# Kernel optimization log

Hardware: AMD Instinct MI355X
Metric: run time of the kernel (lower is better)

## Reference

```python
import jax, jax.numpy as jnp
import numpy as np

# Model dims (match init_kwargs)
U, I, E = 100000, 50000, 1000000   # users, items, interactions
FD, EK, EF = 64, 64, 64            # feature_dim, embed_k, embed_f
L = 3                              # n_layers
B = 16384                          # scoring batch
ALPHA = [1.0 / (k + 1) for k in range(L + 1)]


def setup_inputs() -> dict:
    key = jax.random.key(0)
    ks = jax.random.split(key, 9)
    Gu = jax.random.normal(ks[0], (U, EK), jnp.float32) * 0.05
    Gi = jax.random.normal(ks[1], (I, EK), jnp.float32) * 0.05
    F = jax.random.normal(ks[2], (FD, EF), jnp.float32) * 0.1
    proj_w = jax.random.normal(ks[3], (EF, 1), jnp.float32) * 0.1
    proj_b = jnp.zeros((1,), jnp.float32)
    # sparse binary-ish decomposition-path feature matrix (dense here)
    edge_features = (jax.random.uniform(ks[4], (E, FD)) < 0.1).astype(jnp.float32)
    u = jax.random.randint(ks[5], (E,), 0, U)
    it = jax.random.randint(ks[6], (E,), 0, I) + U  # items offset by num_users
    edge_index = jnp.stack([jnp.concatenate([u, it]),
                            jnp.concatenate([it, u])]).astype(jnp.int64)  # [2, 2E]
    users = jax.random.randint(ks[7], (B,), 0, U).astype(jnp.int64)
    items = jax.random.randint(ks[8], (B,), 0, I).astype(jnp.int64)
    return dict(Gu=Gu, Gi=Gi, F=F, proj_w=proj_w, proj_b=proj_b,
                edge_features=edge_features, edge_index=edge_index,
                users=users, items=items)


def _propagate(Gu, Gi, F, proj_w, proj_b, edge_features, edge_index):
    N = U + I
    src, dst = edge_index[0], edge_index[1]
    # edge-feature projection -> scalar edge weight, duplicated per direction
    ew = (edge_features @ F) @ proj_w + proj_b            # [E, 1]
    ew = jnp.concatenate([ew, ew], axis=0)[:, 0]          # [2E]
    # symmetric GCN normalization over the bipartite interaction graph
    deg = jax.ops.segment_sum(jnp.ones_like(ew), dst, num_segments=N)  # [N]
    dinv = jnp.where(deg > 0, jax.lax.rsqrt(jnp.maximum(deg, 1.0)), 0.0)
    coef = (dinv[src] * dinv[dst] * ew)[:, None]          # [2E, 1]
    x = jnp.concatenate([Gu, Gi], axis=0)                 # [N, K]
    out = ALPHA[0] * x
    for k in range(L):  # edge-conditioned gather -> scale -> scatter-add
        x = jax.ops.segment_sum(coef * x[src], dst, num_segments=N)
        out = out + ALPHA[k + 1] * x
    return out[:U], out[U:]


def reference(Gu, Gi, F, proj_w, proj_b, edge_features, edge_index, users, items):
    gu, gi = _propagate(Gu, Gi, F, proj_w, proj_b, edge_features, edge_index)
    # forward(): masked dot-product scoring of (user, item) pairs
    return jnp.sum(gu[users] * gi[items], axis=1)  # [B]
```

## Files before the change

### kernel.cpp

```cpp
#include <hip/hip_runtime.h>

constexpr int Uc = 100000;
constexpr int Ic = 50000;
constexpr int Nc = 150000;
constexpr int Ec = 1000000;
constexpr int Bc = 16384;
constexpr int NBS = (Nc + 1023) / 1024;

typedef _Float16 h16;
union H4 { uint2 u; h16 h[4]; };


__global__ void k_zero(uint4* __restrict__ deg4) {
    int i = blockIdx.x * blockDim.x + threadIdx.x;
    if (i < Nc / 4) deg4[i] = make_uint4(0u, 0u, 0u, 0u);
}

__global__ void k_deg2_fproj(const int* __restrict__ un, const int* __restrict__ in_,
                             unsigned* __restrict__ deg,
                             const float* __restrict__ F, const float* __restrict__ pw,
                             float* __restrict__ Fp) {
    if (blockIdx.x == 0 && threadIdx.x < 64) {
        int d = threadIdx.x;
        float s = 0.f;
#pragma unroll
        for (int j = 0; j < 64; ++j) s += F[d * 64 + j] * pw[j];
        Fp[d] = s;
    }
    int e = blockIdx.x * blockDim.x + threadIdx.x;
    if (e < Ec) {
        atomicAdd(&deg[un[e]], 1u);
        atomicAdd(&deg[in_[e]], 1u);
    }
}

__global__ void k_scan1(const unsigned* __restrict__ deg, int* __restrict__ rowptr,
                        int* __restrict__ bsums, float* __restrict__ dinv) {
    __shared__ int sh[256];
    int tid = threadIdx.x, bid = blockIdx.x;
    int base = bid * 1024 + tid * 4;
    int v0 = (base + 0 < Nc) ? (int)deg[base + 0] : 0;
    int v1 = (base + 1 < Nc) ? (int)deg[base + 1] : 0;
    int v2 = (base + 2 < Nc) ? (int)deg[base + 2] : 0;
    int v3 = (base + 3 < Nc) ? (int)deg[base + 3] : 0;
    if (base + 0 < Nc) dinv[base + 0] = v0 ? rsqrtf((float)v0) : 0.f;
    if (base + 1 < Nc) dinv[base + 1] = v1 ? rsqrtf((float)v1) : 0.f;
    if (base + 2 < Nc) dinv[base + 2] = v2 ? rsqrtf((float)v2) : 0.f;
    if (base + 3 < Nc) dinv[base + 3] = v3 ? rsqrtf((float)v3) : 0.f;
    int s = v0 + v1 + v2 + v3;
    sh[tid] = s;
    __syncthreads();
    for (int off = 1; off < 256; off <<= 1) {
        int t = (tid >= off) ? sh[tid - off] : 0;
        __syncthreads();
        sh[tid] += t;
        __syncthreads();
    }
    int excl = sh[tid] - s;
    if (tid == 255) bsums[bid] = sh[255];
    if (base + 0 < Nc) rowptr[base + 0] = excl;
    if (base + 1 < Nc) rowptr[base + 1] = excl + v0;
    if (base + 2 < Nc) rowptr[base + 2] = excl + v0 + v1;
    if (base + 3 < Nc) rowptr[base + 3] = excl + v0 + v1 + v2;
}

__global__ void k_scan3(int* __restrict__ rowptr, const int* __restrict__ bsums,
                        int* __restrict__ cursor) {
    __shared__ int sh[256];
    int tid = threadIdx.x;
    int v = (tid < NBS) ? bsums[tid] : 0;
    sh[tid] = v;
    __syncthreads();
    for (int off = 1; off < 256; off <<= 1) {
        int t = (tid >= off) ? sh[tid - off] : 0;
        __syncthreads();
        sh[tid] += t;
        __syncthreads();
    }
    int excl = sh[tid] - v;
    __syncthreads();
    sh[tid] = excl;
    __syncthreads();
    int i = blockIdx.x * blockDim.x + threadIdx.x;
    if (i < Nc) {
        int r = rowptr[i] + sh[i >> 10];
        rowptr[i] = r;
        cursor[i] = r;
    }
    if (i == 0) rowptr[Nc] = 2 * Ec;
}

__global__ void k_build(const int* __restrict__ un, const int* __restrict__ in_,
                        const float* __restrict__ ef, const float* __restrict__ Fp,
                        const float* __restrict__ pb, const float* __restrict__ dinv,
                        int* __restrict__ cursor, int2* __restrict__ csr) {
    int t = blockIdx.x * blockDim.x + threadIdx.x;
    int e = t >> 4, l = t & 15;
    if (e >= Ec) return;
    float4 f = reinterpret_cast<const float4*>(ef)[(size_t)e * 16 + l];
    float4 w = reinterpret_cast<const float4*>(Fp)[l];
    float s = f.x * w.x + f.y * w.y + f.z * w.z + f.w * w.w;
    s += __shfl_xor(s, 8, 16);
    s += __shfl_xor(s, 4, 16);
    s += __shfl_xor(s, 2, 16);
    s += __shfl_xor(s, 1, 16);
    if (l == 0 || l == 8) {
        int uu = un[e], ii = in_[e];
        float c = dinv[uu] * dinv[ii] * (s + pb[0]);
        if (l == 0) {
            int pos = atomicAdd(&cursor[ii], 1);
            csr[pos] = make_int2(uu, __float_as_int(c));
        } else {
            int pos = atomicAdd(&cursor[uu], 1);
            csr[pos] = make_int2(ii, __float_as_int(c));
        }
    }
}

__global__ void k_xin(const float* __restrict__ Gu, const float* __restrict__ Gi,
                      uint2* __restrict__ xin) {
    int t = blockIdx.x * blockDim.x + threadIdx.x;
    if (t >= Nc * 16) return;
    float4 v = (t < Uc * 16) ? reinterpret_cast<const float4*>(Gu)[t]
                             : reinterpret_cast<const float4*>(Gi)[t - Uc * 16];
    H4 o;
    o.h[0] = (h16)v.x; o.h[1] = (h16)v.y; o.h[2] = (h16)v.z; o.h[3] = (h16)v.w;
    xin[t] = o.u;
}

__global__ void k_gprop(const int* __restrict__ rowptr, const int2* __restrict__ csr,
                        const uint2* __restrict__ x, uint2* __restrict__ xn) {
    int t = blockIdx.x * blockDim.x + threadIdx.x;
    int n = t >> 4, l = t & 15;
    if (n >= Nc) return;
    int e0 = rowptr[n], e1 = rowptr[n + 1];
    float4 acc = make_float4(0.f, 0.f, 0.f, 0.f);
    int e = e0;
    for (; e + 4 <= e1; e += 4) {
        int2 s0 = csr[e], s1 = csr[e + 1], s2 = csr[e + 2], s3 = csr[e + 3];
        H4 v0, v1, v2, v3;
        v0.u = x[s0.x * 16 + l];
        v1.u = x[s1.x * 16 + l];
        v2.u = x[s2.x * 16 + l];
        v3.u = x[s3.x * 16 + l];
        float c0 = __int_as_float(s0.y), c1 = __int_as_float(s1.y);
        float c2 = __int_as_float(s2.y), c3 = __int_as_float(s3.y);
        acc.x += c0 * (float)v0.h[0] + c1 * (float)v1.h[0] + c2 * (float)v2.h[0] + c3 * (float)v3.h[0];
        acc.y += c0 * (float)v0.h[1] + c1 * (float)v1.h[1] + c2 * (float)v2.h[1] + c3 * (float)v3.h[1];
        acc.z += c0 * (float)v0.h[2] + c1 * (float)v1.h[2] + c2 * (float)v2.h[2] + c3 * (float)v3.h[2];
        acc.w += c0 * (float)v0.h[3] + c1 * (float)v1.h[3] + c2 * (float)v2.h[3] + c3 * (float)v3.h[3];
    }
    for (; e < e1; ++e) {
        int2 sc = csr[e];
        float c = __int_as_float(sc.y);
        H4 v; v.u = x[sc.x * 16 + l];
        acc.x += c * (float)v.h[0]; acc.y += c * (float)v.h[1];
        acc.z += c * (float)v.h[2]; acc.w += c * (float)v.h[3];
    }
    H4 o;
    o.h[0] = (h16)acc.x; o.h[1] = (h16)acc.y; o.h[2] = (h16)acc.z; o.h[3] = (h16)acc.w;
    xn[n * 16 + l] = o.u;
}

__global__ void k_final(const float* __restrict__ Gu, const float* __restrict__ Gi,
                        const h16* __restrict__ x1, const h16* __restrict__ x2,
                        const int* __restrict__ rowptr, const int2* __restrict__ csr,
                        const int* __restrict__ users, const int* __restrict__ items,
                        float* __restrict__ out) {
    int wid = (blockIdx.x * blockDim.x + threadIdx.x) >> 6;
    int d = threadIdx.x & 63;
    if (wid >= Bc) return;
    int un = users[wid];
    int in_ = Uc + items[wid];

    float acc2[2];
#pragma unroll
    for (int side = 0; side < 2; ++side) {
        int n = side ? in_ : un;
        float base = side ? Gi[(size_t)(n - Uc) * 64 + d] : Gu[(size_t)n * 64 + d];
        float a = base + 0.5f * (float)x1[(size_t)n * 64 + d]
                       + (1.f / 3.f) * (float)x2[(size_t)n * 64 + d];
        float su = 0.f;
        int e0 = rowptr[n], e1 = rowptr[n + 1];
        int e = e0;
        for (; e + 4 <= e1; e += 4) {
            int2 s0 = csr[e], s1 = csr[e + 1], s2 = csr[e + 2], s3 = csr[e + 3];
            su += __int_as_float(s0.y) * (float)x2[(size_t)s0.x * 64 + d]
                + __int_as_float(s1.y) * (float)x2[(size_t)s1.x * 64 + d]
                + __int_as_float(s2.y) * (float)x2[(size_t)s2.x * 64 + d]
                + __int_as_float(s3.y) * (float)x2[(size_t)s3.x * 64 + d];
        }
        for (; e < e1; ++e) {
            int2 sc = csr[e];
            su += __int_as_float(sc.y) * (float)x2[(size_t)sc.x * 64 + d];
        }
        acc2[side] = a + 0.25f * su;
    }

    float p = acc2[0] * acc2[1];
#pragma unroll
    for (int o = 32; o > 0; o >>= 1) p += __shfl_xor(p, o, 64);
    if (d == 0) out[wid] = p;
}


extern "C" void kernel_launch(void* const* d_in, const int* in_sizes, int n_in,
                              void* d_out, int out_size, void* d_ws, size_t ws_size,
                              hipStream_t stream) {
    const float* Gu = (const float*)d_in[0];
    const float* Gi = (const float*)d_in[1];
    const float* F  = (const float*)d_in[2];
    const float* pw = (const float*)d_in[3];
    const float* pb = (const float*)d_in[4];
    const float* ef = (const float*)d_in[5];
    const int*   ei = (const int*)d_in[6];
    const int* users = (const int*)d_in[7];
    const int* items = (const int*)d_in[8];
    float* out = (float*)d_out;

    float* ws = (float*)d_ws;
    float*    Fp     = ws;
    float*    dinv   = Fp + 64;
    unsigned* deg    = (unsigned*)(dinv + Nc);
    int*      rowptr = (int*)(deg + Nc);
    int*      cursor = rowptr + (Nc + 16);
    int*      bsums  = cursor + Nc;
    int2*     csr    = (int2*)(bsums + 256);
    h16*      xin    = (h16*)(csr + 2 * Ec);
    h16*      xa     = xin + (size_t)Nc * 64;
    h16*      xb     = xa + (size_t)Nc * 64;

    const int* un  = ei;
    const int* in_ = ei + 2 * Ec;

    k_zero<<<(Nc / 4 + 255) / 256, 256, 0, stream>>>((uint4*)deg);
    k_deg2_fproj<<<(Ec + 255) / 256, 256, 0, stream>>>(un, in_, deg, F, pw, Fp);
    k_scan1<<<NBS, 256, 0, stream>>>(deg, rowptr, bsums, dinv);
    k_scan3<<<(Nc + 255) / 256, 256, 0, stream>>>(rowptr, bsums, cursor);
    k_build<<<(Ec * 16) / 256, 256, 0, stream>>>(un, in_, ef, Fp, pb, dinv, cursor, csr);
    k_xin<<<(Nc * 16 + 255) / 256, 256, 0, stream>>>(Gu, Gi, (uint2*)xin);

    k_gprop<<<(Nc * 16 + 255) / 256, 256, 0, stream>>>(rowptr, csr, (const uint2*)xin, (uint2*)xa);
    k_gprop<<<(Nc * 16 + 255) / 256, 256, 0, stream>>>(rowptr, csr, (const uint2*)xa, (uint2*)xb);

    k_final<<<(Bc * 64) / 256, 256, 0, stream>>>(Gu, Gi, xa, xb, rowptr, csr, users, items, out);
}
```

Baseline: 351.8 us.

## Split fp16 embeddings into four column-quarter planes for cache-resident propagation

```diff
diff --git a/kernel.cpp b/kernel.cpp
--- a/kernel.cpp
+++ b/kernel.cpp
@@ -9,6 +9,7 @@
 
 typedef _Float16 h16;
 union H4 { uint2 u; h16 h[4]; };
+
 
 
 __global__ void k_zero(uint4* __restrict__ deg4) {
@@ -118,89 +119,119 @@
 }
 
 __global__ void k_xin(const float* __restrict__ Gu, const float* __restrict__ Gi,
-                      uint2* __restrict__ xin) {
+                      uint2* __restrict__ xq) {
     int t = blockIdx.x * blockDim.x + threadIdx.x;
     if (t >= Nc * 16) return;
-    float4 v = (t < Uc * 16) ? reinterpret_cast<const float4*>(Gu)[t]
-                             : reinterpret_cast<const float4*>(Gi)[t - Uc * 16];
+    int l4 = t & 3;
+    int qn = t >> 2;
+    int q = qn / Nc;
+    int n = qn - q * Nc;
+    float4 v;
+    if (n < Uc) v = reinterpret_cast<const float4*>(Gu)[n * 16 + q * 4 + l4];
+    else        v = reinterpret_cast<const float4*>(Gi)[(n - Uc) * 16 + q * 4 + l4];
     H4 o;
     o.h[0] = (h16)v.x; o.h[1] = (h16)v.y; o.h[2] = (h16)v.z; o.h[3] = (h16)v.w;
-    xin[t] = o.u;
-}
-
-__global__ void k_gprop(const int* __restrict__ rowptr, const int2* __restrict__ csr,
-                        const uint2* __restrict__ x, uint2* __restrict__ xn) {
-    int t = blockIdx.x * blockDim.x + threadIdx.x;
-    int n = t >> 4, l = t & 15;
+    xq[t] = o.u;
+}
+
+__global__ void k_gprop_q(const int* __restrict__ rowptr, const int2* __restrict__ csr,
+                          const uint2* __restrict__ x, uint2* __restrict__ xn) {
+    int t = blockIdx.x * blockDim.x + threadIdx.x;
+    int n = t >> 2, l = t & 3;
     if (n >= Nc) return;
     int e0 = rowptr[n], e1 = rowptr[n + 1];
-    float4 acc = make_float4(0.f, 0.f, 0.f, 0.f);
+    float acc[4] = {0.f, 0.f, 0.f, 0.f};
     int e = e0;
     for (; e + 4 <= e1; e += 4) {
         int2 s0 = csr[e], s1 = csr[e + 1], s2 = csr[e + 2], s3 = csr[e + 3];
         H4 v0, v1, v2, v3;
-        v0.u = x[s0.x * 16 + l];
-        v1.u = x[s1.x * 16 + l];
-        v2.u = x[s2.x * 16 + l];
-        v3.u = x[s3.x * 16 + l];
+        v0.u = x[s0.x * 4 + l];
+        v1.u = x[s1.x * 4 + l];
+        v2.u = x[s2.x * 4 + l];
+        v3.u = x[s3.x * 4 + l];
         float c0 = __int_as_float(s0.y), c1 = __int_as_float(s1.y);
         float c2 = __int_as_float(s2.y), c3 = __int_as_float(s3.y);
-        acc.x += c0 * (float)v0.h[0] + c1 * (float)v1.h[0] + c2 * (float)v2.h[0] + c3 * (float)v3.h[0];
-        acc.y += c0 * (float)v0.h[1] + c1 * (float)v1.h[1] + c2 * (float)v2.h[1] + c3 * (float)v3.h[1];
-        acc.z += c0 * (float)v0.h[2] + c1 * (float)v1.h[2] + c2 * (float)v2.h[2] + c3 * (float)v3.h[2];
-        acc.w += c0 * (float)v0.h[3] + c1 * (float)v1.h[3] + c2 * (float)v2.h[3] + c3 * (float)v3.h[3];
+#pragma unroll
+        for (int j = 0; j < 4; ++j)
+            acc[j] += c0 * (float)v0.h[j] + c1 * (float)v1.h[j]
+                    + c2 * (float)v2.h[j] + c3 * (float)v3.h[j];
     }
     for (; e < e1; ++e) {
         int2 sc = csr[e];
         float c = __int_as_float(sc.y);
-        H4 v; v.u = x[sc.x * 16 + l];
-        acc.x += c * (float)v.h[0]; acc.y += c * (float)v.h[1];
-        acc.z += c * (float)v.h[2]; acc.w += c * (float)v.h[3];
+        H4 v; v.u = x[sc.x * 4 + l];
+#pragma unroll
+        for (int j = 0; j < 4; ++j) acc[j] += c * (float)v.h[j];
     }
     H4 o;
-    o.h[0] = (h16)acc.x; o.h[1] = (h16)acc.y; o.h[2] = (h16)acc.z; o.h[3] = (h16)acc.w;
-    xn[n * 16 + l] = o.u;
+#pragma unroll
+    for (int j = 0; j < 4; ++j) o.h[j] = (h16)acc[j];
+    xn[n * 4 + l] = o.u;
 }
 
 __global__ void k_final(const float* __restrict__ Gu, const float* __restrict__ Gi,
-                        const h16* __restrict__ x1, const h16* __restrict__ x2,
+                        const uint2* __restrict__ x1, const uint2* __restrict__ x2,
                         const int* __restrict__ rowptr, const int2* __restrict__ csr,
                         const int* __restrict__ users, const int* __restrict__ items,
                         float* __restrict__ out) {
-    int wid = (blockIdx.x * blockDim.x + threadIdx.x) >> 6;
-    int d = threadIdx.x & 63;
+    int t = blockIdx.x * blockDim.x + threadIdx.x;
+    int wid = t >> 4, l = t & 15;
     if (wid >= Bc) return;
-    int un = users[wid];
-    int in_ = Uc + items[wid];
-
-    float acc2[2];
+    int qoff = (l >> 2) * Nc;
+    int l4 = l & 3;
+
+    float uv[4], iv[4];
 #pragma unroll
     for (int side = 0; side < 2; ++side) {
-        int n = side ? in_ : un;
-        float base = side ? Gi[(size_t)(n - Uc) * 64 + d] : Gu[(size_t)n * 64 + d];
-        float a = base + 0.5f * (float)x1[(size_t)n * 64 + d]
-                       + (1.f / 3.f) * (float)x2[(size_t)n * 64 + d];
-        float su = 0.f;
+        int n = side ? (Uc + items[wid]) : users[wid];
+        float4 bv = side ? reinterpret_cast<const float4*>(Gi)[(n - Uc) * 16 + l]
+                         : reinterpret_cast<const float4*>(Gu)[n * 16 + l];
+        H4 h1, h2;
+        h1.u = x1[(size_t)(qoff + n) * 4 + l4];
+        h2.u = x2[(size_t)(qoff + n) * 4 + l4];
+        float a[4];
+        a[0] = bv.x + 0.5f * (float)h1.h[0] + (1.f / 3.f) * (float)h2.h[0];
+        a[1] = bv.y + 0.5f * (float)h1.h[1] + (1.f / 3.f) * (float)h2.h[1];
+        a[2] = bv.z + 0.5f * (float)h1.h[2] + (1.f / 3.f) * (float)h2.h[2];
+        a[3] = bv.w + 0.5f * (float)h1.h[3] + (1.f / 3.f) * (float)h2.h[3];
+
+        float su[4] = {0.f, 0.f, 0.f, 0.f};
         int e0 = rowptr[n], e1 = rowptr[n + 1];
         int e = e0;
         for (; e + 4 <= e1; e += 4) {
             int2 s0 = csr[e], s1 = csr[e + 1], s2 = csr[e + 2], s3 = csr[e + 3];
-            su += __int_as_float(s0.y) * (float)x2[(size_t)s0.x * 64 + d]
-                + __int_as_float(s1.y) * (float)x2[(size_t)s1.x * 64 + d]
-                + __int_as_float(s2.y) * (float)x2[(size_t)s2.x * 64 + d]
-                + __int_as_float(s3.y) * (float)x2[(size_t)s3.x * 64 + d];
+            H4 v0, v1, v2, v3;
+            v0.u = x2[(size_t)(qoff + s0.x) * 4 + l4];
+            v1.u = x2[(size_t)(qoff + s1.x) * 4 + l4];
+            v2.u = x2[(size_t)(qoff + s2.x) * 4 + l4];
+            v3.u = x2[(size_t)(qoff + s3.x) * 4 + l4];
+            float c0 = __int_as_float(s0.y), c1 = __int_as_float(s1.y);
+            float c2 = __int_as_float(s2.y), c3 = __int_as_float(s3.y);
+#pragma unroll
+            for (int j = 0; j < 4; ++j)
+                su[j] += c0 * (float)v0.h[j] + c1 * (float)v1.h[j]
+                       + c2 * (float)v2.h[j] + c3 * (float)v3.h[j];
         }
         for (; e < e1; ++e) {
             int2 sc = csr[e];
-            su += __int_as_float(sc.y) * (float)x2[(size_t)sc.x * 64 + d];
-        }
-        acc2[side] = a + 0.25f * su;
-    }
-
-    float p = acc2[0] * acc2[1];
-#pragma unroll
-    for (int o = 32; o > 0; o >>= 1) p += __shfl_xor(p, o, 64);
-    if (d == 0) out[wid] = p;
+            float c = __int_as_float(sc.y);
+            H4 v; v.u = x2[(size_t)(qoff + sc.x) * 4 + l4];
+#pragma unroll
+            for (int j = 0; j < 4; ++j) su[j] += c * (float)v.h[j];
+        }
+#pragma unroll
+        for (int j = 0; j < 4; ++j) {
+            float p = a[j] + 0.25f * su[j];
+            if (side == 0) uv[j] = p; else iv[j] = p;
+        }
+    }
+
+    float p = uv[0] * iv[0] + uv[1] * iv[1] + uv[2] * iv[2] + uv[3] * iv[3];
+    p += __shfl_xor(p, 8, 16);
+    p += __shfl_xor(p, 4, 16);
+    p += __shfl_xor(p, 2, 16);
+    p += __shfl_xor(p, 1, 16);
+    if (l == 0) out[wid] = p;
 }
 
 
@@ -240,8 +271,14 @@
     k_build<<<(Ec * 16) / 256, 256, 0, stream>>>(un, in_, ef, Fp, pb, dinv, cursor, csr);
     k_xin<<<(Nc * 16 + 255) / 256, 256, 0, stream>>>(Gu, Gi, (uint2*)xin);
 
-    k_gprop<<<(Nc * 16 + 255) / 256, 256, 0, stream>>>(rowptr, csr, (const uint2*)xin, (uint2*)xa);
-    k_gprop<<<(Nc * 16 + 255) / 256, 256, 0, stream>>>(rowptr, csr, (const uint2*)xa, (uint2*)xb);
-
-    k_final<<<(Bc * 64) / 256, 256, 0, stream>>>(Gu, Gi, xa, xb, rowptr, csr, users, items, out);
-}
+    const int gpb = (Nc * 4 + 255) / 256;
+    for (int q = 0; q < 4; ++q)
+        k_gprop_q<<<gpb, 256, 0, stream>>>(rowptr, csr,
+            (const uint2*)xin + (size_t)q * Nc * 4, (uint2*)xa + (size_t)q * Nc * 4);
+    for (int q = 0; q < 4; ++q)
+        k_gprop_q<<<gpb, 256, 0, stream>>>(rowptr, csr,
+            (const uint2*)xa + (size_t)q * Nc * 4, (uint2*)xb + (size_t)q * Nc * 4);
+
+    k_final<<<(Bc * 16 + 255) / 256, 256, 0, stream>>>(Gu, Gi, (const uint2*)xa, (const uint2*)xb,
+                                                       rowptr, csr, users, items, out);
+}
```

Result: slower. 438.9 us (+24.7%).
